# Performance work log

Hardware: AMD Instinct MI355X
Metric: run time of the kernel (lower is better)

The kernel has to match this reference:

```python
import jax, jax.numpy as jnp
import numpy as np

DIM = 1024
HEADS = 8
HEAD_DIM = DIM // HEADS
D_STATE = 256
BATCH = 8192
DT_MIN = 1e-3
DT_MAX = 1e-1
EPS = 1e-4  # RMSNorm eps


def setup_inputs() -> dict:
    key = jax.random.key(0)
    ks = jax.random.split(key, 8)
    x_t = jax.random.normal(ks[0], (BATCH, DIM), dtype=jnp.float32)
    state_re = jax.random.normal(ks[1], (BATCH, HEADS, D_STATE), dtype=jnp.float32)
    state_im = jax.random.normal(ks[2], (BATCH, HEADS, D_STATE), dtype=jnp.float32)
    # parameters (match torch init)
    norm_weight = jnp.ones((DIM,), dtype=jnp.float32)
    A_re_log = jnp.full((HEADS, D_STATE), float(np.log(0.5)), dtype=jnp.float32)
    n = jnp.arange(1, D_STATE + 1, dtype=jnp.float32)
    A_im = jnp.broadcast_to(float(np.pi) * n, (HEADS, D_STATE)).astype(jnp.float32)
    b_scale = 1.0 / float(np.sqrt(HEAD_DIM))
    c_scale = 1.0 / float(np.sqrt(D_STATE))
    B_re = jax.random.normal(ks[3], (HEADS, D_STATE, HEAD_DIM), dtype=jnp.float32) * b_scale
    B_im = jax.random.normal(ks[4], (HEADS, D_STATE, HEAD_DIM), dtype=jnp.float32) * b_scale
    C_re = jax.random.normal(ks[5], (HEADS, HEAD_DIM, D_STATE), dtype=jnp.float32) * c_scale
    C_im = jax.random.normal(ks[6], (HEADS, HEAD_DIM, D_STATE), dtype=jnp.float32) * c_scale
    D = jnp.ones((DIM,), dtype=jnp.float32)
    # log_dt: inverse-softplus of log-uniform dt in [dt_min, dt_max]
    u = jax.random.uniform(ks[7], (HEADS, D_STATE), dtype=jnp.float32)
    dt = jnp.exp(u * (np.log(DT_MAX) - np.log(DT_MIN)) + np.log(DT_MIN))
    dt = jnp.maximum(dt, 1e-4)
    log_dt = dt + jnp.log(-jnp.expm1(-dt))
    return dict(x_t=x_t, state_re=state_re, state_im=state_im,
                norm_weight=norm_weight, A_re_log=A_re_log, A_im=A_im,
                B_re=B_re, B_im=B_im, C_re=C_re, C_im=C_im, D=D, log_dt=log_dt)


def reference(x_t, state_re, state_im, norm_weight, A_re_log, A_im,
              B_re, B_im, C_re, C_im, D, log_dt):
    batch = x_t.shape[0]
    # RMSNorm (eps=1e-4, elementwise affine)
    ms = jnp.mean(jnp.square(x_t), axis=-1, keepdims=True)
    x = x_t * jax.lax.rsqrt(ms + EPS) * norm_weight
    x_h = x.reshape(batch, HEADS, HEAD_DIM)  # (B,H,P)
    # discretize
    A = jax.lax.complex(-jnp.exp(A_re_log), A_im)            # (H,N)
    dt = jax.nn.softplus(log_dt)                              # (H,N)
    A_bar = jnp.exp(dt.astype(A.dtype) * A)                   # (H,N) complex
    B = jax.lax.complex(B_re, B_im)                           # (H,N,P)
    C = jax.lax.complex(C_re, C_im)                           # (H,P,N)
    B_bar = ((A_bar - 1.0) / A)[..., None] * B                # (H,N,P)
    # recurrent step
    state = jax.lax.complex(state_re, state_im)               # (B,H,N)
    Bx = jnp.einsum('hnp,bhp->bhn', B_bar, x_h.astype(B_bar.dtype))
    new_state = A_bar[None] * state + Bx                      # (B,H,N)
    Ch = jnp.einsum('hpn,bhn->bhp', C, new_state)             # (B,H,P)
    D_h = D.reshape(HEADS, HEAD_DIM)[None]                    # (1,H,P)
    y_h = 2.0 * Ch.real + D_h * x_h
    out = x_t + y_h.reshape(batch, DIM)
    return out, new_state.real, new_state.imag
```

## Files before the change

### kernel.cpp

```cpp
#include <hip/hip_runtime.h>

#define BATCH 8192
#define DIM 1024
#define HEADS 8
#define HEAD_DIM 128
#define DSTATE 256

typedef __attribute__((ext_vector_type(8))) short short8v;
typedef __attribute__((ext_vector_type(4))) float f32x4;
typedef __attribute__((ext_vector_type(4))) unsigned short ushort4v;
typedef __attribute__((ext_vector_type(4))) unsigned int uint4v;

__device__ __forceinline__ unsigned short f2bf(float x) {
  unsigned int u = __builtin_bit_cast(unsigned int, x);
  unsigned int r = u + 0x7FFFu + ((u >> 16) & 1u);
  return (unsigned short)(r >> 16);
}
__device__ __forceinline__ float bf2f(unsigned short h) {
  unsigned int u = ((unsigned int)h) << 16;
  return __builtin_bit_cast(float, u);
}

__device__ __forceinline__ void stage16f(const float* g, float* l) {
  __builtin_amdgcn_global_load_lds(
      (const __attribute__((address_space(1))) unsigned int*)g,
      (__attribute__((address_space(3))) unsigned int*)l, 16, 0, 0);
}
__device__ __forceinline__ void stage4u(const unsigned short* g, unsigned short* l) {
  __builtin_amdgcn_global_load_lds(
      (const __attribute__((address_space(1))) unsigned int*)g,
      (__attribute__((address_space(3))) unsigned int*)l, 4, 0, 0);
}

#define BARRIER() do { \
  asm volatile("s_waitcnt lgkmcnt(0)" ::: "memory"); \
  __builtin_amdgcn_s_barrier(); \
  asm volatile("" ::: "memory"); } while (0)


__global__ __launch_bounds__(256) void prep(
    const float* __restrict__ logdt, const float* __restrict__ arelog,
    const float* __restrict__ aim,
    const float* __restrict__ Bre, const float* __restrict__ Bim,
    const float* __restrict__ Cre, const float* __restrict__ Cim,
    const float* __restrict__ xtg, const float* __restrict__ normw,
    unsigned short* __restrict__ w1re, unsigned short* __restrict__ w1im,
    unsigned short* __restrict__ w2re, unsigned short* __restrict__ w2mi,
    float* __restrict__ abr, float* __restrict__ abi,
    float* __restrict__ scale, unsigned short* __restrict__ xtb) {
  const int blk = blockIdx.x;
  if (blk < 1024) {
    const int i = blk * 256 + threadIdx.x;
    const int p = i & 127, s = (i >> 7) & 255, h = i >> 15;
    const int kk = s >> 4, u = s & 15;
    const int n = ((kk >> 1) << 5) + ((u >> 2) & 3) * 8 + (kk & 1) * 4 + (u & 3);
    const int hn = h * 256 + n;
    const float ld = logdt[hn];
    const float dt = log1pf(expf(ld));
    const float Ar = -expf(arelog[hn]);
    const float Ai = aim[hn];
    const float e = expf(dt * Ar), th = dt * Ai;
    const float Abr = e * cosf(th), Abi = e * sinf(th);
    if (p == 0) { abr[h * 256 + s] = Abr; abi[h * 256 + s] = Abi; }
    const float den = Ar * Ar + Ai * Ai;
    const float br_ = Abr - 1.0f;
    const float cr = (br_ * Ar + Abi * Ai) / den;
    const float ci = (Abi * Ar - br_ * Ai) / den;
    const int src = hn * 128 + p;
    const float wb = normw[h * 128 + p];
    const float bre = Bre[src], bim = Bim[src];
    w1re[i] = f2bf((cr * bre - ci * bim) * wb);
    w1im[i] = f2bf((cr * bim + ci * bre) * wb);
  } else if (blk < 2048) {
    const int i = (blk - 1024) * 256 + threadIdx.x;
    w2re[i] = f2bf(Cre[i]);
    w2mi[i] = f2bf(-Cim[i]);
  } else {
    const int wid = threadIdx.x >> 6, lane = threadIdx.x & 63;
    const int row = (blk - 2048) * 4 + wid;
    const float* xr = xtg + (size_t)row * DIM;
    unsigned short* xo = xtb + (size_t)row * DIM;
    float ssq = 0.f;
    #pragma unroll
    for (int c = 0; c < 4; ++c) {
      const f32x4 v = *(const f32x4*)(xr + c * 256 + lane * 4);
      ssq += v[0]*v[0] + v[1]*v[1] + v[2]*v[2] + v[3]*v[3];
      ushort4v o;
      o[0] = f2bf(v[0]); o[1] = f2bf(v[1]); o[2] = f2bf(v[2]); o[3] = f2bf(v[3]);
      *(ushort4v*)(xo + c * 256 + lane * 4) = o;
    }
    #pragma unroll
    for (int m = 1; m < 64; m <<= 1) ssq += __shfl_xor(ssq, m, 64);
    if (lane == 0) scale[row] = rsqrtf(ssq * (1.0f / DIM) + 1e-4f);
  }
}

__global__ __launch_bounds__(512, 2) void s5_main(
    const unsigned short* __restrict__ w1re, const unsigned short* __restrict__ w1im,
    const unsigned short* __restrict__ w2re, const unsigned short* __restrict__ w2mi,
    const float* __restrict__ abrp, const float* __restrict__ abip,
    const float* __restrict__ scale, const unsigned short* __restrict__ xtb,
    const float* __restrict__ sre, const float* __restrict__ sim,
    const float* __restrict__ dvec, const float* __restrict__ normw,
    float* __restrict__ out, float* __restrict__ nsre, float* __restrict__ nsim) {
  __shared__ float Sb[4][2][16][256];
  __shared__ unsigned short xbL[4][16][128];
  __shared__ float scL[256];
  const int tid = threadIdx.x;
  const int w = tid >> 6, lane = tid & 63;
  const int g = lane >> 4, bl = lane & 15;
  const int h = blockIdx.x & 7;
  const int blkrow = (blockIdx.x >> 3) * 256;

  short8v w1r[2][4], w1i[2][4];
  #pragma unroll
  for (int t = 0; t < 2; ++t) {
    const int kk = 2 * w + t;
    const unsigned short* pr = w1re + ((size_t)(h * DSTATE + kk * 16 + bl)) * HEAD_DIM + g * 8;
    const unsigned short* pi = w1im + ((size_t)(h * DSTATE + kk * 16 + bl)) * HEAD_DIM + g * 8;
    #pragma unroll
    for (int ks = 0; ks < 4; ++ks) {
      w1r[t][ks] = *(const short8v*)(pr + ks * 32);
      w1i[t][ks] = *(const short8v*)(pi + ks * 32);
    }
  }
  short8v w2r[8], w2i[8];
  {
    const unsigned short* qr = w2re + ((size_t)(h * HEAD_DIM + w * 16 + bl)) * DSTATE + g * 8;
    const unsigned short* qi = w2mi + ((size_t)(h * HEAD_DIM + w * 16 + bl)) * DSTATE + g * 8;
    #pragma unroll
    for (int j = 0; j < 8; ++j) {
      w2r[j] = *(const short8v*)(qr + j * 32);
      w2i[j] = *(const short8v*)(qi + j * 32);
    }
  }
  f32x4 Arh[2], Aih[2];
  #pragma unroll
  for (int t = 0; t < 2; ++t) {
    Arh[t] = *(const f32x4*)(abrp + h * DSTATE + (2 * w + t) * 16 + g * 4);
    Aih[t] = *(const f32x4*)(abip + h * DSTATE + (2 * w + t) * 16 + g * 4);
  }
  f32x4 d4;
  {
    const int col = h * HEAD_DIM + w * 16 + g * 4;
    const f32x4 dv = *(const f32x4*)(dvec + col);
    const f32x4 nv = *(const f32x4*)(normw + col);
    #pragma unroll
    for (int r = 0; r < 4; ++r) d4[r] = dv[r] * nv[r];
  }

  auto STAGE = [&](int t, int b) {
    const int gr0 = blkrow + t * 16;
    #pragma unroll
    for (int i = 0; i < 2; ++i) {
      const int row = 2 * w + i;
      const size_t rb = ((size_t)(gr0 + row) * HEADS + h) * DSTATE;
      const int soff = (lane ^ (row & 7)) * 4;
      stage16f(sre + rb + soff, &Sb[b][0][row][0]);
      stage16f(sim + rb + soff, &Sb[b][1][row][0]);
    }
    #pragma unroll
    for (int i = 0; i < 2; ++i) {
      const int row = 2 * w + i;
      const unsigned short* src = xtb + (size_t)(gr0 + row) * DIM + h * HEAD_DIM
          + (((lane >> 2) ^ (row & 7)) << 3) + ((lane & 3) << 1);
      stage4u(src, &xbL[b][row][0]);
    }
  };

  auto PHASE1 = [&](int t) {
    const int b = t & 3;
    const float scl = scL[t * 16 + bl];
    short8v xf[4];
    #pragma unroll
    for (int ks = 0; ks < 4; ++ks) {
      const int ch = (ks * 4 + g) ^ (bl & 7);
      uint4v u = *(const uint4v*)&xbL[b][bl][ch * 8];
      uint4v o;
      #pragma unroll
      for (int q = 0; q < 4; ++q) {
        const float lo = bf2f((unsigned short)(u[q] & 0xffffu)) * scl;
        const float hi = bf2f((unsigned short)(u[q] >> 16)) * scl;
        o[q] = (unsigned)f2bf(lo) | ((unsigned)f2bf(hi) << 16);
      }
      xf[ks] = __builtin_bit_cast(short8v, o);
    }
    #pragma unroll
    for (int tt = 0; tt < 2; ++tt) {
      f32x4 dr = {0.f,0.f,0.f,0.f};
      f32x4 di = {0.f,0.f,0.f,0.f};
      #pragma unroll
      for (int ks = 0; ks < 4; ++ks)
        dr = __builtin_amdgcn_mfma_f32_16x16x32_bf16(w1r[tt][ks], xf[ks], dr, 0, 0, 0);
      #pragma unroll
      for (int ks = 0; ks < 4; ++ks)
        di = __builtin_amdgcn_mfma_f32_16x16x32_bf16(w1i[tt][ks], xf[ks], di, 0, 0, 0);
      const int c = (((8 * w + 2 * g + tt) ^ (bl & 7)) << 2);
      const f32x4 s_r = *(const f32x4*)&Sb[b][0][bl][c];
      const f32x4 s_i = *(const f32x4*)&Sb[b][1][bl][c];
      f32x4 nr, ni;
      #pragma unroll
      for (int r = 0; r < 4; ++r) {
        nr[r] = fmaf(Arh[tt][r], s_r[r], fmaf(-Aih[tt][r], s_i[r], dr[r]));
        ni[r] = fmaf(Arh[tt][r], s_i[r], fmaf(Aih[tt][r], s_r[r], di[r]));
      }
      *(f32x4*)&Sb[b][0][bl][c] = nr;
      *(f32x4*)&Sb[b][1][bl][c] = ni;
    }
  };

  auto PHASE2 = [&](int t) {
    const int b = t & 3;
    #pragma unroll
    for (int i = 0; i < 2; ++i) {
      const int row = 2 * w + i;
      const size_t rb = ((size_t)(blkrow + t * 16 + row) * HEADS + h) * DSTATE;
      const int gc = (lane ^ (row & 7)) * 4;
      const f32x4 vr = *(const f32x4*)&Sb[b][0][row][lane * 4];
      const f32x4 vi = *(const f32x4*)&Sb[b][1][row][lane * 4];
      __builtin_nontemporal_store(vr, (f32x4*)(nsre + rb + gc));
      __builtin_nontemporal_store(vi, (f32x4*)(nsim + rb + gc));
    }
    f32x4 a2 = {0.f,0.f,0.f,0.f};
    #pragma unroll
    for (int j = 0; j < 8; ++j) {
      const int c0 = (((8 * j + 2 * g)     ^ (bl & 7)) << 2);
      const int c1 = (((8 * j + 2 * g + 1) ^ (bl & 7)) << 2);
      const f32x4 r0 = *(const f32x4*)&Sb[b][0][bl][c0];
      const f32x4 r1 = *(const f32x4*)&Sb[b][0][bl][c1];
      const f32x4 i0 = *(const f32x4*)&Sb[b][1][bl][c0];
      const f32x4 i1 = *(const f32x4*)&Sb[b][1][bl][c1];
      uint4v ur, ui;
      ur[0] = (unsigned)f2bf(r0[0]) | ((unsigned)f2bf(r0[1]) << 16);
      ur[1] = (unsigned)f2bf(r0[2]) | ((unsigned)f2bf(r0[3]) << 16);
      ur[2] = (unsigned)f2bf(r1[0]) | ((unsigned)f2bf(r1[1]) << 16);
      ur[3] = (unsigned)f2bf(r1[2]) | ((unsigned)f2bf(r1[3]) << 16);
      ui[0] = (unsigned)f2bf(i0[0]) | ((unsigned)f2bf(i0[1]) << 16);
      ui[1] = (unsigned)f2bf(i0[2]) | ((unsigned)f2bf(i0[3]) << 16);
      ui[2] = (unsigned)f2bf(i1[0]) | ((unsigned)f2bf(i1[1]) << 16);
      ui[3] = (unsigned)f2bf(i1[2]) | ((unsigned)f2bf(i1[3]) << 16);
      const short8v pbr = __builtin_bit_cast(short8v, ur);
      const short8v pbi = __builtin_bit_cast(short8v, ui);
      a2 = __builtin_amdgcn_mfma_f32_16x16x32_bf16(w2r[j], pbr, a2, 0, 0, 0);
      a2 = __builtin_amdgcn_mfma_f32_16x16x32_bf16(w2i[j], pbi, a2, 0, 0, 0);
    }
    const float scl = scL[t * 16 + bl];
    const int col = h * HEAD_DIM + w * 16 + g * 4;
    const size_t o = (size_t)(blkrow + t * 16 + bl) * DIM + col;
    const unsigned short* xp =
        &xbL[b][bl][((((2 * w) + (g >> 1)) ^ (bl & 7)) << 3) + ((g & 1) << 2)];
    f32x4 ro;
    #pragma unroll
    for (int r = 0; r < 4; ++r) {
      const float xr = bf2f(xp[r]);
      ro[r] = xr * (1.0f + d4[r] * scl) + 2.0f * a2[r];
    }
    __builtin_nontemporal_store(ro, (f32x4*)(out + o));
  };

  if (w == 0) stage16f(scale + blkrow + lane * 4, &scL[0]);
  STAGE(0, 0);
  STAGE(1, 1);
  asm volatile("s_waitcnt vmcnt(6)" ::: "memory");

  for (int t = 0; t < 16; ++t) {
    if (t == 1)                asm volatile("s_waitcnt vmcnt(6)"  ::: "memory");
    else if (t == 2)           asm volatile("s_waitcnt vmcnt(11)" ::: "memory");
    else if (t >= 3 && t <= 14) asm volatile("s_waitcnt vmcnt(16)" ::: "memory");
    else if (t == 15)          asm volatile("s_waitcnt vmcnt(10)" ::: "memory");
    BARRIER();
    if (t + 2 < 16) STAGE(t + 2, (t + 2) & 3);
    __builtin_amdgcn_sched_barrier(0);
    if (t > 0) PHASE2(t - 1);
    PHASE1(t);
  }
  BARRIER();
  PHASE2(15);
}

extern "C" void kernel_launch(void* const* d_in, const int* in_sizes, int n_in,
                              void* d_out, int out_size, void* d_ws, size_t ws_size,
                              hipStream_t stream) {
  const float* x_t      = (const float*)d_in[0];
  const float* state_re = (const float*)d_in[1];
  const float* state_im = (const float*)d_in[2];
  const float* norm_w   = (const float*)d_in[3];
  const float* A_re_log = (const float*)d_in[4];
  const float* A_im     = (const float*)d_in[5];
  const float* B_re     = (const float*)d_in[6];
  const float* B_im     = (const float*)d_in[7];
  const float* C_re     = (const float*)d_in[8];
  const float* C_im     = (const float*)d_in[9];
  const float* Dv       = (const float*)d_in[10];
  const float* log_dt   = (const float*)d_in[11];

  float* out   = (float*)d_out;
  float* ns_re = out + (size_t)BATCH * DIM;
  float* ns_im = ns_re + (size_t)BATCH * HEADS * DSTATE;

  char* ws = (char*)d_ws;
  unsigned short* w1re = (unsigned short*)ws;
  unsigned short* w1im = w1re + 262144;
  unsigned short* w2re = w1im + 262144;
  unsigned short* w2mi = w2re + 262144;
  float* abr   = (float*)(ws + 4 * 524288);
  float* abi   = abr + 2048;
  float* scale = abi + 2048;
  unsigned short* xtb = (unsigned short*)(scale + 8192);

  prep<<<4096, 256, 0, stream>>>(log_dt, A_re_log, A_im, B_re, B_im, C_re, C_im,
                                 x_t, norm_w, w1re, w1im, w2re, w2mi,
                                 abr, abi, scale, xtb);
  s5_main<<<256, 512, 0, stream>>>(w1re, w1im, w2re, w2mi, abr, abi, scale, xtb,
                                   state_re, state_im, Dv, norm_w,
                                   out, ns_re, ns_im);
}
```

Before: 96.21 us.

## Pack new state to bf16 in phase one and write state directly from registers

Phase one now converts the updated complex state to bf16 once and writes it into a small dedicated LDS buffer laid out as MFMA operands. It also stores the fp32 new state to global memory directly from registers, using cross-lane shuffles to form contiguous vectors. Phase two no longer rereads fp32 state from LDS or repeats the conversion, and the ring buffer shrinks from four stages to three, cutting LDS use. In exchange, each iteration adds a barrier between the phases, removes the overlap of phase two for tile t-1 with phase one for tile t, and adds many shuffles plus retuned vmcnt waits.

```diff
diff --git a/kernel.cpp b/kernel.cpp
--- a/kernel.cpp
+++ b/kernel.cpp
@@ -103,8 +103,9 @@
     const float* __restrict__ sre, const float* __restrict__ sim,
     const float* __restrict__ dvec, const float* __restrict__ normw,
     float* __restrict__ out, float* __restrict__ nsre, float* __restrict__ nsim) {
-  __shared__ float Sb[4][2][16][256];
-  __shared__ unsigned short xbL[4][16][128];
+  __shared__ float Sb[3][2][16][256];
+  __shared__ unsigned short xbL[3][16][128];
+  __shared__ unsigned short pf[2][8][64][8];
   __shared__ float scL[256];
   const int tid = threadIdx.x;
   const int w = tid >> 6, lane = tid & 63;
@@ -148,6 +149,8 @@
     #pragma unroll
     for (int r = 0; r < 4; ++r) d4[r] = dv[r] * nv[r];
   }
+  const int srcA = ((g >> 1) << 4) + bl;
+  const int srcB = (((g >> 1) + 2) << 4) + bl;
 
   auto STAGE = [&](int t, int b) {
     const int gr0 = blkrow + t * 16;
@@ -169,7 +172,7 @@
   };
 
   auto PHASE1 = [&](int t) {
-    const int b = t & 3;
+    const int b = t % 3;
     const float scl = scL[t * 16 + bl];
     short8v xf[4];
     #pragma unroll
@@ -185,6 +188,8 @@
       }
       xf[ks] = __builtin_bit_cast(short8v, o);
     }
+    f32x4 nre[2], nim[2];
+    unsigned pr0 = 0, pr1 = 0, pi0 = 0, pi1 = 0;
     #pragma unroll
     for (int tt = 0; tt < 2; ++tt) {
       f32x4 dr = {0.f,0.f,0.f,0.f};
@@ -204,43 +209,49 @@
         nr[r] = fmaf(Arh[tt][r], s_r[r], fmaf(-Aih[tt][r], s_i[r], dr[r]));
         ni[r] = fmaf(Arh[tt][r], s_i[r], fmaf(Aih[tt][r], s_r[r], di[r]));
       }
-      *(f32x4*)&Sb[b][0][bl][c] = nr;
-      *(f32x4*)&Sb[b][1][bl][c] = ni;
-    }
+      nre[tt] = nr; nim[tt] = ni;
+      unsigned lo  = (unsigned)f2bf(nr[0]) | ((unsigned)f2bf(nr[1]) << 16);
+      unsigned hi  = (unsigned)f2bf(nr[2]) | ((unsigned)f2bf(nr[3]) << 16);
+      unsigned lo2 = (unsigned)f2bf(ni[0]) | ((unsigned)f2bf(ni[1]) << 16);
+      unsigned hi2 = (unsigned)f2bf(ni[2]) | ((unsigned)f2bf(ni[3]) << 16);
+      if (tt == 0) { pr0 = lo; pr1 = hi; pi0 = lo2; pi1 = hi2; }
+      else {
+        uint4v urv; urv[0] = pr0; urv[1] = pr1; urv[2] = lo;  urv[3] = hi;
+        uint4v uiv; uiv[0] = pi0; uiv[1] = pi1; uiv[2] = lo2; uiv[3] = hi2;
+        *(short8v*)&pf[0][w][lane][0] = __builtin_bit_cast(short8v, urv);
+        *(short8v*)&pf[1][w][lane][0] = __builtin_bit_cast(short8v, uiv);
+      }
+    }
+    f32x4 v1r, v2r, v1i, v2i;
+    #pragma unroll
+    for (int e = 0; e < 4; ++e) {
+      float a1 = __shfl(nre[0][e], srcA, 64);
+      float b1 = __shfl(nre[1][e], srcA, 64);
+      v1r[e] = (g & 1) ? b1 : a1;
+      float a2 = __shfl(nre[0][e], srcB, 64);
+      float b2 = __shfl(nre[1][e], srcB, 64);
+      v2r[e] = (g & 1) ? b2 : a2;
+      float c1 = __shfl(nim[0][e], srcA, 64);
+      float d1 = __shfl(nim[1][e], srcA, 64);
+      v1i[e] = (g & 1) ? d1 : c1;
+      float c2 = __shfl(nim[0][e], srcB, 64);
+      float d2 = __shfl(nim[1][e], srcB, 64);
+      v2i[e] = (g & 1) ? d2 : c2;
+    }
+    const size_t no = ((size_t)(blkrow + t * 16 + bl) * HEADS + h) * DSTATE + w * 32 + g * 4;
+    __builtin_nontemporal_store(v1r, (f32x4*)(nsre + no));
+    __builtin_nontemporal_store(v2r, (f32x4*)(nsre + no + 16));
+    __builtin_nontemporal_store(v1i, (f32x4*)(nsim + no));
+    __builtin_nontemporal_store(v2i, (f32x4*)(nsim + no + 16));
   };
 
   auto PHASE2 = [&](int t) {
-    const int b = t & 3;
-    #pragma unroll
-    for (int i = 0; i < 2; ++i) {
-      const int row = 2 * w + i;
-      const size_t rb = ((size_t)(blkrow + t * 16 + row) * HEADS + h) * DSTATE;
-      const int gc = (lane ^ (row & 7)) * 4;
-      const f32x4 vr = *(const f32x4*)&Sb[b][0][row][lane * 4];
-      const f32x4 vi = *(const f32x4*)&Sb[b][1][row][lane * 4];
-      __builtin_nontemporal_store(vr, (f32x4*)(nsre + rb + gc));
-      __builtin_nontemporal_store(vi, (f32x4*)(nsim + rb + gc));
-    }
+    const int b = t % 3;
     f32x4 a2 = {0.f,0.f,0.f,0.f};
     #pragma unroll
     for (int j = 0; j < 8; ++j) {
-      const int c0 = (((8 * j + 2 * g)     ^ (bl & 7)) << 2);
-      const int c1 = (((8 * j + 2 * g + 1) ^ (bl & 7)) << 2);
-      const f32x4 r0 = *(const f32x4*)&Sb[b][0][bl][c0];
-      const f32x4 r1 = *(const f32x4*)&Sb[b][0][bl][c1];
-      const f32x4 i0 = *(const f32x4*)&Sb[b][1][bl][c0];
-      const f32x4 i1 = *(const f32x4*)&Sb[b][1][bl][c1];
-      uint4v ur, ui;
-      ur[0] = (unsigned)f2bf(r0[0]) | ((unsigned)f2bf(r0[1]) << 16);
-      ur[1] = (unsigned)f2bf(r0[2]) | ((unsigned)f2bf(r0[3]) << 16);
-      ur[2] = (unsigned)f2bf(r1[0]) | ((unsigned)f2bf(r1[1]) << 16);
-      ur[3] = (unsigned)f2bf(r1[2]) | ((unsigned)f2bf(r1[3]) << 16);
-      ui[0] = (unsigned)f2bf(i0[0]) | ((unsigned)f2bf(i0[1]) << 16);
-      ui[1] = (unsigned)f2bf(i0[2]) | ((unsigned)f2bf(i0[3]) << 16);
-      ui[2] = (unsigned)f2bf(i1[0]) | ((unsigned)f2bf(i1[1]) << 16);
-      ui[3] = (unsigned)f2bf(i1[2]) | ((unsigned)f2bf(i1[3]) << 16);
-      const short8v pbr = __builtin_bit_cast(short8v, ur);
-      const short8v pbi = __builtin_bit_cast(short8v, ui);
+      const short8v pbr = *(const short8v*)&pf[0][j][lane][0];
+      const short8v pbi = *(const short8v*)&pf[1][j][lane][0];
       a2 = __builtin_amdgcn_mfma_f32_16x16x32_bf16(w2r[j], pbr, a2, 0, 0, 0);
       a2 = __builtin_amdgcn_mfma_f32_16x16x32_bf16(w2i[j], pbi, a2, 0, 0, 0);
     }
@@ -261,21 +272,19 @@
   if (w == 0) stage16f(scale + blkrow + lane * 4, &scL[0]);
   STAGE(0, 0);
   STAGE(1, 1);
-  asm volatile("s_waitcnt vmcnt(6)" ::: "memory");
 
   for (int t = 0; t < 16; ++t) {
-    if (t == 1)                asm volatile("s_waitcnt vmcnt(6)"  ::: "memory");
-    else if (t == 2)           asm volatile("s_waitcnt vmcnt(11)" ::: "memory");
-    else if (t >= 3 && t <= 14) asm volatile("s_waitcnt vmcnt(16)" ::: "memory");
-    else if (t == 15)          asm volatile("s_waitcnt vmcnt(10)" ::: "memory");
+    if (t == 0)      asm volatile("s_waitcnt vmcnt(6)"  ::: "memory");
+    else if (t == 1) asm volatile("s_waitcnt vmcnt(11)" ::: "memory");
+    else if (t <= 14) asm volatile("s_waitcnt vmcnt(16)" ::: "memory");
+    else             asm volatile("s_waitcnt vmcnt(10)" ::: "memory");
     BARRIER();
-    if (t + 2 < 16) STAGE(t + 2, (t + 2) & 3);
+    if (t + 2 < 16) STAGE(t + 2, (t + 2) % 3);
     __builtin_amdgcn_sched_barrier(0);
-    if (t > 0) PHASE2(t - 1);
     PHASE1(t);
-  }
-  BARRIER();
-  PHASE2(15);
+    BARRIER();
+    PHASE2(t);
+  }
 }
 
 extern "C" void kernel_launch(void* const* d_in, const int* in_sizes, int n_in,
```

New measurement: 91.15 us. 1.06x faster.
